# Performance work log

Measured on AMD Instinct MI355X. Metric: run time of the kernel, lower is better.

The kernel has to match this reference:

```python
import jax, jax.numpy as jnp
import numpy as np


def _margins(labels):
    # labels: [B, L] int. Imposter index j = roll(i+1, wrap).
    lab_j = jnp.roll(labels, -1, axis=0)
    equal = jnp.all(labels == lab_j, axis=1)                 # [B]
    n = jnp.sum(labels | lab_j, axis=1).astype(jnp.float32)  # union count
    diff = jnp.sum(labels ^ lab_j, axis=1).astype(jnp.float32)
    margin = jnp.maximum(0.5, diff / jnp.maximum(n, 1.0))
    return jnp.where(equal, 0.0, margin)                     # [B]


def setup_inputs() -> dict:
    key = jax.random.key(0)
    k1, k2, k3 = jax.random.split(key, 3)
    B, D, L = 16384, 512, 14
    z_image = jax.random.normal(k1, (B, D), dtype=jnp.float32)
    z_text = jax.random.normal(k2, (B, D), dtype=jnp.float32)
    labels = jax.random.randint(k3, (B, L), 0, 2, dtype=jnp.int32)
    return {"z_image": z_image, "z_text": z_text, "labels": labels}


def reference(z_image, z_text, labels):
    # similarity_function='dot' (default in forward call sites)
    B = z_image.shape[0]
    margin = _margins(labels)                                 # [B]
    paired = jnp.sum(z_image * z_text, axis=1)                # [B] dot(z_image[i], z_text[i])
    zi_j = jnp.roll(z_image, -1, axis=0)                      # z_image[j]
    zt_j = jnp.roll(z_text, -1, axis=0)                       # z_text[j]
    imp_img = jnp.sum(zi_j * z_text, axis=1)                  # dot(z_image[j], z_text[i])
    imp_txt = jnp.sum(zt_j * z_image, axis=1)                 # dot(z_text[j], z_image[i])
    loss_img = jnp.sum(jnp.maximum(imp_img - paired + margin, 0.0)) / B
    loss_txt = jnp.sum(jnp.maximum(imp_txt - paired + margin, 0.0)) / B
    return (loss_img + loss_txt).reshape(1)
```

## Files before the change

kernel.cpp:

```cpp
#include <hip/hip_runtime.h>


constexpr int B = 16384;
constexpr int D = 512;
constexpr int L = 14;
constexpr int BLOCK = 256;
constexpr int WAVES_PER_BLOCK = BLOCK / 64;
constexpr int ROWS_PER_WAVE = 2;
constexpr int GRID = B / (WAVES_PER_BLOCK * ROWS_PER_WAVE);

__global__ __launch_bounds__(BLOCK) void rank_loss_kernel(
    const float* __restrict__ zi, const float* __restrict__ zt,
    const int* __restrict__ labels, float* __restrict__ out)
{
    const int lane = threadIdx.x & 63;
    const int wv   = threadIdx.x >> 6;
    const int gw   = blockIdx.x * WAVES_PER_BLOCK + wv;

    float acc = 0.0f;

    #pragma unroll
    for (int r = 0; r < ROWS_PER_WAVE; ++r) {
        const int i = gw * ROWS_PER_WAVE + r;
        const int j = (i + 1) & (B - 1);

        const float4* zi_i = (const float4*)(zi + (size_t)i * D);
        const float4* zt_i = (const float4*)(zt + (size_t)i * D);
        const float4* zi_j = (const float4*)(zi + (size_t)j * D);
        const float4* zt_j = (const float4*)(zt + (size_t)j * D);

        float pd = 0.0f, pii = 0.0f, pit = 0.0f;
        #pragma unroll
        for (int c = 0; c < 2; ++c) {
            const int idx = lane + 64 * c;
            const float4 a  = zi_i[idx];
            const float4 b  = zt_i[idx];
            const float4 aj = zi_j[idx];
            const float4 bj = zt_j[idx];
            pd  += a.x * b.x + a.y * b.y + a.z * b.z + a.w * b.w;
            pii += aj.x * b.x + aj.y * b.y + aj.z * b.z + aj.w * b.w;
            pit += bj.x * a.x + bj.y * a.y + bj.z * a.z + bj.w * a.w;
        }

        int pk = 0;
        if (lane < L) {
            const int a  = labels[i * L + lane];
            const int bv = labels[j * L + lane];
            pk = (a | bv) | ((a ^ bv) << 8) | ((int)(a != bv) << 16);
        }

        #pragma unroll
        for (int off = 32; off > 0; off >>= 1) {
            pd  += __shfl_down(pd,  off);
            pii += __shfl_down(pii, off);
            pit += __shfl_down(pit, off);
            pk  += __shfl_down(pk,  off);
        }

        if (lane == 0) {
            const int n    = pk & 0xff;
            const int diff = (pk >> 8) & 0xff;
            const int neq  = (pk >> 16) & 0xff;
            float margin;
            if (neq == 0) {
                margin = 0.0f;
            } else {
                margin = fmaxf(0.5f, (float)diff / fmaxf((float)n, 1.0f));
            }
            acc += fmaxf(pii - pd + margin, 0.0f)
                 + fmaxf(pit - pd + margin, 0.0f);
        }
    }

    __shared__ float s[WAVES_PER_BLOCK];
    if (lane == 0) s[wv] = acc;
    __syncthreads();
    if (threadIdx.x == 0) {
        float t = 0.0f;
        #pragma unroll
        for (int w = 0; w < WAVES_PER_BLOCK; ++w) t += s[w];
        atomicAdd(out, t * (1.0f / (float)B));
    }
}

extern "C" void kernel_launch(void* const* d_in, const int* in_sizes, int n_in,
                              void* d_out, int out_size, void* d_ws, size_t ws_size,
                              hipStream_t stream) {
    const float* zi     = (const float*)d_in[0];
    const float* zt     = (const float*)d_in[1];
    const int*   labels = (const int*)d_in[2];
    float* out = (float*)d_out;

    hipMemsetAsync(out, 0, sizeof(float), stream);
    rank_loss_kernel<<<GRID, BLOCK, 0, stream>>>(zi, zt, labels, out);
}
```

Before: 116.3 us.

## Reuse neighbour row across consecutive rows per wave and use two-pass reduction

Each wave now processes eight consecutive rows and keeps the next row's image/text vectors and labels in registers so they become the current row in the next iteration, roughly halving global reads. Label union/xor counts are computed with wave ballots and popcount instead of shuffle-reducing a packed integer. The float atomic plus memset is replaced by per-block partials in workspace and a separate single-block reduce kernel. This trades fewer blocks in flight and an extra launch for reduced memory traffic and deterministic summation.

```diff
diff --git a/kernel.cpp b/kernel.cpp
--- a/kernel.cpp
+++ b/kernel.cpp
@@ -5,82 +5,90 @@
 constexpr int D = 512;
 constexpr int L = 14;
 constexpr int BLOCK = 256;
-constexpr int WAVES_PER_BLOCK = BLOCK / 64;
-constexpr int ROWS_PER_WAVE = 2;
-constexpr int GRID = B / (WAVES_PER_BLOCK * ROWS_PER_WAVE);
+constexpr int WPB = BLOCK / 64;
+constexpr int R = 8;
+constexpr int GRID = B / (WPB * R);
 
-__global__ __launch_bounds__(BLOCK) void rank_loss_kernel(
+__device__ __forceinline__ float dot4(float4 a, float4 b) {
+    return a.x * b.x + a.y * b.y + a.z * b.z + a.w * b.w;
+}
+
+__global__ __launch_bounds__(BLOCK) void rank_main(
     const float* __restrict__ zi, const float* __restrict__ zt,
-    const int* __restrict__ labels, float* __restrict__ out)
+    const int* __restrict__ labels, float* __restrict__ ws)
 {
     const int lane = threadIdx.x & 63;
     const int wv   = threadIdx.x >> 6;
-    const int gw   = blockIdx.x * WAVES_PER_BLOCK + wv;
+    const int gw   = blockIdx.x * WPB + wv;
+    const int base = gw * R;
+
+    const float4* zi4 = (const float4*)zi;
+    const float4* zt4 = (const float4*)zt;
+
+    size_t o = (size_t)base * 128 + lane;
+    float4 a0 = zi4[o], a1 = zi4[o + 64];
+    float4 b0 = zt4[o], b1 = zt4[o + 64];
+    int lab = (lane < L) ? labels[base * L + lane] : 0;
+    float pd = dot4(a0, b0) + dot4(a1, b1);
 
     float acc = 0.0f;
 
     #pragma unroll
-    for (int r = 0; r < ROWS_PER_WAVE; ++r) {
-        const int i = gw * ROWS_PER_WAVE + r;
-        const int j = (i + 1) & (B - 1);
+    for (int r = 0; r < R; ++r) {
+        const int nrow = (base + r + 1) & (B - 1);
+        const size_t no = (size_t)nrow * 128 + lane;
+        const float4 na0 = zi4[no], na1 = zi4[no + 64];
+        const float4 nb0 = zt4[no], nb1 = zt4[no + 64];
+        const int nlab = (lane < L) ? labels[nrow * L + lane] : 0;
 
-        const float4* zi_i = (const float4*)(zi + (size_t)i * D);
-        const float4* zt_i = (const float4*)(zt + (size_t)i * D);
-        const float4* zi_j = (const float4*)(zi + (size_t)j * D);
-        const float4* zt_j = (const float4*)(zt + (size_t)j * D);
+        float pii = dot4(na0, b0) + dot4(na1, b1);
+        float pit = dot4(nb0, a0) + dot4(nb1, a1);
+        float npd = dot4(na0, nb0) + dot4(na1, nb1);
 
-        float pd = 0.0f, pii = 0.0f, pit = 0.0f;
-        #pragma unroll
-        for (int c = 0; c < 2; ++c) {
-            const int idx = lane + 64 * c;
-            const float4 a  = zi_i[idx];
-            const float4 b  = zt_i[idx];
-            const float4 aj = zi_j[idx];
-            const float4 bj = zt_j[idx];
-            pd  += a.x * b.x + a.y * b.y + a.z * b.z + a.w * b.w;
-            pii += aj.x * b.x + aj.y * b.y + aj.z * b.z + aj.w * b.w;
-            pit += bj.x * a.x + bj.y * a.y + bj.z * a.z + bj.w * a.w;
-        }
+        const unsigned long long bor  = __ballot((lab | nlab) != 0);
+        const unsigned long long bxor = __ballot((lab ^ nlab) != 0);
 
-        int pk = 0;
-        if (lane < L) {
-            const int a  = labels[i * L + lane];
-            const int bv = labels[j * L + lane];
-            pk = (a | bv) | ((a ^ bv) << 8) | ((int)(a != bv) << 16);
-        }
-
+        float s0 = pd, s1 = pii, s2 = pit;
         #pragma unroll
         for (int off = 32; off > 0; off >>= 1) {
-            pd  += __shfl_down(pd,  off);
-            pii += __shfl_down(pii, off);
-            pit += __shfl_down(pit, off);
-            pk  += __shfl_down(pk,  off);
+            s0 += __shfl_down(s0, off);
+            s1 += __shfl_down(s1, off);
+            s2 += __shfl_down(s2, off);
         }
 
         if (lane == 0) {
-            const int n    = pk & 0xff;
-            const int diff = (pk >> 8) & 0xff;
-            const int neq  = (pk >> 16) & 0xff;
-            float margin;
-            if (neq == 0) {
-                margin = 0.0f;
-            } else {
-                margin = fmaxf(0.5f, (float)diff / fmaxf((float)n, 1.0f));
+            const int df = __popcll(bxor);
+            float margin = 0.0f;
+            if (df != 0) {
+                const int n = __popcll(bor);
+                margin = fmaxf(0.5f, (float)df / (float)n);
             }
-            acc += fmaxf(pii - pd + margin, 0.0f)
-                 + fmaxf(pit - pd + margin, 0.0f);
+            acc += fmaxf(s1 - s0 + margin, 0.0f)
+                 + fmaxf(s2 - s0 + margin, 0.0f);
         }
+
+        a0 = na0; a1 = na1; b0 = nb0; b1 = nb1;
+        lab = nlab; pd = npd;
     }
 
-    __shared__ float s[WAVES_PER_BLOCK];
+    __shared__ float s[WPB];
     if (lane == 0) s[wv] = acc;
     __syncthreads();
-    if (threadIdx.x == 0) {
-        float t = 0.0f;
-        #pragma unroll
-        for (int w = 0; w < WAVES_PER_BLOCK; ++w) t += s[w];
-        atomicAdd(out, t * (1.0f / (float)B));
-    }
+    if (threadIdx.x == 0)
+        ws[blockIdx.x] = s[0] + s[1] + s[2] + s[3];
+}
+
+__global__ __launch_bounds__(BLOCK) void rank_reduce(
+    const float* __restrict__ ws, float* __restrict__ out)
+{
+    float v = ws[threadIdx.x] + ws[threadIdx.x + BLOCK];
+    #pragma unroll
+    for (int off = 32; off > 0; off >>= 1) v += __shfl_down(v, off);
+    __shared__ float s[WPB];
+    if ((threadIdx.x & 63) == 0) s[threadIdx.x >> 6] = v;
+    __syncthreads();
+    if (threadIdx.x == 0)
+        out[0] = (s[0] + s[1] + s[2] + s[3]) * (1.0f / (float)B);
 }
 
 extern "C" void kernel_launch(void* const* d_in, const int* in_sizes, int n_in,
@@ -90,7 +98,8 @@
     const float* zt     = (const float*)d_in[1];
     const int*   labels = (const int*)d_in[2];
     float* out = (float*)d_out;
+    float* ws  = (float*)d_ws;
 
-    hipMemsetAsync(out, 0, sizeof(float), stream);
-    rank_loss_kernel<<<GRID, BLOCK, 0, stream>>>(zi, zt, labels, out);
+    rank_main<<<GRID, BLOCK, 0, stream>>>(zi, zt, labels, ws);
+    rank_reduce<<<1, BLOCK, 0, stream>>>(ws, out);
 }
```

New measurement: 99.23 us. 14.7% less time.
